# Optimization experiments

Measured on AMD Instinct MI355X. Metric: run time of the kernel, lower is better.

The kernel has to match this reference:

```python
import jax, jax.numpy as jnp
import numpy as np

IN_C, OUT_C, K, UP, C_DIM = 128, 64, 3, 2, 512
CLAMP = 256.0
ACT_GAIN = np.sqrt(2.0)  # lrelu def_gain


def _upfirdn_up2(x, f2):
    """upfirdn2d with up=2, padding=(3,2,3,2), gain=up^2 for a 4-tap filter.

    Padding values come from conv2d_resample: p = k//2 = 1, fw = 4, up = 2 =>
    px0 = p + (fw+up-1)//2 = 3, px1 = p + (fw-up)//2 = 2.
    """
    N, C, H, W = x.shape
    px0, px1 = 3, 2
    # zero-insert upsample (interior padding) fused with edge padding;
    # trailing zero of the up-sampled signal folded into the high pad.
    x = jax.lax.pad(x, jnp.asarray(0, x.dtype),
                    ((0, 0, 0), (0, 0, 0),
                     (px0, px1 + (UP - 1), UP - 1),
                     (px0, px1 + (UP - 1), UP - 1)))
    k = (f2 * (UP * UP)).astype(x.dtype)[None, None]   # [1,1,4,4], symmetric -> flip is a no-op
    k = jnp.tile(k, (C, 1, 1, 1))                       # depthwise FIR
    return jax.lax.conv_general_dilated(
        x, k, window_strides=(1, 1), padding='VALID',
        feature_group_count=C, dimension_numbers=('NCHW', 'OIHW', 'NCHW'))


def setup_inputs() -> dict:
    key = jax.random.key(0)
    ks = jax.random.split(key, 4)
    return {
        "x": jax.random.normal(ks[0], (8, IN_C, 128, 128), jnp.float32),
        "c": jax.random.normal(ks[1], (8, C_DIM), jnp.float32),
        "weight": jax.random.normal(ks[2], (OUT_C, IN_C, K, K), jnp.float32),
        "bias": jnp.zeros((OUT_C,), jnp.float32),
        "w_affine": jax.random.normal(ks[3], (IN_C, C_DIM), jnp.float32),
        "b_affine": jnp.zeros((IN_C,), jnp.float32),
    }


def reference(x, c, weight, bias, w_affine, b_affine):
    # setup_filter: normalize separable FIR taps
    f1 = jnp.array([1.0, 3.0, 3.0, 1.0], jnp.float32)
    f1 = f1 / jnp.sum(f1)
    f2 = jnp.outer(f1, f1)

    # hyper modulation: x *= 1 + tanh(affine(c))
    y = c @ (w_affine * (1.0 / np.sqrt(C_DIM))).T + b_affine   # FullyConnectedLayer, linear
    x = x * (1.0 + jnp.tanh(y))[:, :, None, None]

    # conv2d_resample(up=2, padding=k//2, flip_weight=False)
    w = weight * (1.0 / np.sqrt(IN_C * K * K))                  # weight_gain
    x = _upfirdn_up2(x, f2)                                      # [N,C,2H+2,2W+2]
    w = w[:, :, ::-1, ::-1]                                      # flip_weight=False => true convolution
    x = jax.lax.conv_general_dilated(
        x, w.astype(x.dtype), window_strides=(1, 1), padding='VALID',
        dimension_numbers=('NCHW', 'OIHW', 'NCHW'))              # [N,OUT_C,2H,2W]

    # bias_act: lrelu(x+b)*sqrt(2), clamp at +-256 (gain=1)
    x = jax.nn.leaky_relu(x + bias[None, :, None, None], 0.2) * ACT_GAIN
    return jnp.clip(x, -CLAMP, CLAMP)
```

## Files before the change

### kernel.cpp

```cpp
#include <hip/hip_runtime.h>
#include <math.h>

#define IN_C   128
#define OUT_C  64
#define CDIM   512
#define HW     128
#define PHW    130
#define OHW    256
#define NB     8

typedef __attribute__((ext_vector_type(8))) short short8;
typedef __attribute__((ext_vector_type(4))) float f32x4;

__device__ inline unsigned short f2bf(float f) {
    unsigned int u = __float_as_uint(f);
    unsigned int r = (u + 0x7fffu + ((u >> 16) & 1u)) >> 16;
    return (unsigned short)r;
}

__device__ inline float postact(float v) {
    v = v > 0.f ? v : 0.2f * v;
    v *= 1.4142135623730951f;
    return fminf(fmaxf(v, -256.f), 256.f);
}

__device__ __forceinline__ void gload16(const void* g, void* l) {
    __builtin_amdgcn_global_load_lds(
        (const __attribute__((address_space(1))) unsigned int*)g,
        (__attribute__((address_space(3))) unsigned int*)l, 16, 0, 0);
}

__global__ void gain_kernel(const float* __restrict__ c,
                            const float* __restrict__ w_affine,
                            const float* __restrict__ b_affine,
                            float* __restrict__ gain) {
    int wave = (blockIdx.x * blockDim.x + threadIdx.x) >> 6;
    int lane = threadIdx.x & 63;
    if (wave >= NB * IN_C) return;
    int n  = wave >> 7;
    int ic = wave & 127;
    const float* cp = c + n * CDIM;
    const float* wp = w_affine + ic * CDIM;
    float s = 0.f;
    #pragma unroll
    for (int k = 0; k < CDIM / 64; ++k) s += cp[lane + 64 * k] * wp[lane + 64 * k];
    #pragma unroll
    for (int off = 32; off > 0; off >>= 1) s += __shfl_down(s, off);
    if (lane == 0) {
        float y = s * 0.04419417382415922f + b_affine[ic];
        gain[n * IN_C + ic] = 1.0f + tanhf(y);
    }
}

__global__ void wbprep2_kernel(const float* __restrict__ w, unsigned short* __restrict__ wb2) {
    int idx = blockIdx.x * blockDim.x + threadIdx.x;
    if (idx >= 18 * 16384) return;
    int e    = idx & 7;
    int lane = (idx >> 3) & 63;
    int m16  = (idx >> 9) & 15;
    int kc   = (idx >> 13) & 1;
    int kt   = idx >> 14;
    int tap = kt >> 1, h = kt & 1;
    int m  = m16 * 16 + (lane & 15);
    int ic = h * 64 + kc * 32 + (lane >> 4) * 8 + e;
    int ky = tap / 3, kx = tap % 3;
    int oc = m >> 2, ph = m & 3;
    int py = ph >> 1, px = ph & 1;
    int sy = 2 * ky + (py == 0 ? 1 : 0);
    int sx = 2 * kx + (px == 0 ? 1 : 0);
    const float k1[4] = {0.25f, 0.75f, 0.75f, 0.25f};
    float sum = 0.f;
    #pragma unroll
    for (int by = 0; by < 3; ++by) {
        int ay = sy - by;
        if (ay < 0 || ay > 3) continue;
        #pragma unroll
        for (int bx = 0; bx < 3; ++bx) {
            int ax = sx - bx;
            if (ax < 0 || ax > 3) continue;
            sum += w[((oc * IN_C + ic) * 3 + (2 - by)) * 3 + (2 - bx)] * k1[ay] * k1[ax];
        }
    }
    wb2[idx] = f2bf(sum * 0.029462782549439483f);
}

__global__ __launch_bounds__(256) void xprep_kernel(const float* __restrict__ x,
                                                    const float* __restrict__ gain,
                                                    unsigned short* __restrict__ xg) {
    int n = blockIdx.x >> 7;
    int y = blockIdx.x & 127;
    __shared__ unsigned short lds[128][130];
    int tid = threadIdx.x;
    for (int i = tid; i < 128 * 128; i += 256) {
        int ic = i >> 7, pix = i & 127;
        float v = x[(((n * IN_C + ic) * HW) + y) * HW + pix] * gain[n * IN_C + ic];
        lds[pix][ic] = f2bf(v);
    }
    __syncthreads();
    unsigned int* dst = (unsigned int*)(xg + (((size_t)(n * PHW) + y + 1) * PHW + 1) * 128);
    for (int i = tid; i < 8192; i += 256) {
        int pix = i >> 6, d = i & 63;
        dst[pix * 64 + d] = *reinterpret_cast<const unsigned int*>(&lds[pix][d * 2]);
    }
}

__global__ void border_kernel(unsigned short* __restrict__ xg) {
    int id = blockIdx.x * blockDim.x + threadIdx.x;
    int c = id & 15;
    int t = id >> 4;
    int p = t % 516;
    int n = t / 516;
    if (n >= NB) return;
    int Y, X;
    if (p < 130)      { Y = 0;   X = p; }
    else if (p < 260) { Y = 129; X = p - 130; }
    else              { int q = p - 260; Y = 1 + (q >> 1); X = (q & 1) * 129; }
    uint4 z = make_uint4(0, 0, 0, 0);
    *reinterpret_cast<uint4*>(xg + (((size_t)(n * PHW) + Y) * PHW + X) * 128 + c * 8) = z;
}

#define BARRIER() do { __builtin_amdgcn_sched_barrier(0); __builtin_amdgcn_s_barrier(); __builtin_amdgcn_sched_barrier(0); } while (0)
#define MM(ACC, AF, BF) ACC = __builtin_amdgcn_mfma_f32_16x16x32_bf16(AF, BF, ACC, 0, 0, 0)

__global__ __launch_bounds__(512) void conv_mfma2(
    const unsigned short* __restrict__ xg,
    const unsigned short* __restrict__ wb2,
    const float* __restrict__ bias,
    float* __restrict__ out) {
    __shared__ __align__(16) char smem[131072];

    const int bid = blockIdx.x;
    const int n     = bid >> 6;
    const int patch = bid & 63;
    const int y0 = (patch >> 3) * 16;
    const int x0 = (patch & 7) * 16;
    const int tid  = threadIdx.x;
    const int lane = tid & 63;
    const int wid  = tid >> 6;
    const int wM = wid >> 2;
    const int wN = wid & 3;
    const int l16 = lane & 15;
    const int lhi = lane >> 4;
    const int mbase = wM * 8;
    const int pbase = wN * 4;

    int ldsoff[4]; int aoff[4]; size_t boff[4];
    #pragma unroll
    for (int r = 0; r < 4; ++r) {
        int slot = r * 512 + tid;
        ldsoff[r] = (r * 512 + wid * 64) * 16;
        aoff[r] = slot * 8;
        int px = slot >> 3, j = slot & 7, s = j ^ (px & 7);
        boff[r] = (((size_t)(n * PHW) + y0 + (px >> 4)) * PHW + (x0 + (px & 15))) * 128 + s * 8;
    }

    auto stage = [&](int k, int p) {
        int tap = k >> 1, h = k & 1;
        int ky = tap / 3, kx = tap - ky * 3;
        int toff = (ky * PHW + kx) * 128 + h * 64;
        const unsigned short* aS = wb2 + k * 16384;
        char* bufA = smem + (p << 16);
        #pragma unroll
        for (int r = 0; r < 4; ++r) gload16(aS + aoff[r], bufA + ldsoff[r]);
        #pragma unroll
        for (int r = 0; r < 4; ++r) gload16(xg + boff[r] + toff, bufA + 32768 + ldsoff[r]);
    };

    f32x4 acc[8][4];
    #pragma unroll
    for (int f = 0; f < 8; ++f)
        #pragma unroll
        for (int b = 0; b < 4; ++b) acc[f][b] = (f32x4)0.f;

    stage(0, 0);
    stage(1, 1);

    #pragma unroll 1
    for (int t = 0; t < 18; ++t) {
        const int p = t & 1;
        const char* bA = smem + (p << 16);
        const char* bB = bA + 32768;

        if (t >= 1 && t < 17) stage(t + 1, (t + 1) & 1);
        if (t < 17) { asm volatile("s_waitcnt vmcnt(8)" ::: "memory"); }
        else        { asm volatile("s_waitcnt vmcnt(0)" ::: "memory"); }
        BARRIER();

        auto ldA = [&](int f, int kc) -> short8 {
            return *reinterpret_cast<const short8*>(bA + (((kc << 4) + mbase + f) << 10) + (lane << 4));
        };
        auto ldB = [&](int b, int kc) -> short8 {
            int px = ((pbase + b) << 4) + l16;
            int off = (((kc << 6) + (lhi << 4)) ^ ((px & 7) << 4));
            return *reinterpret_cast<const short8*>(bB + (px << 7) + off);
        };

        short8 A0[4][2], A1[4][2], B0[2][2], B1[2][2];

        #pragma unroll
        for (int f = 0; f < 4; ++f) { A0[f][0] = ldA(f, 0); A0[f][1] = ldA(f, 1); }
        #pragma unroll
        for (int b = 0; b < 2; ++b) { B0[b][0] = ldB(b, 0); B0[b][1] = ldB(b, 1); }
        BARRIER();
        __builtin_amdgcn_s_setprio(1);
        #pragma unroll
        for (int f = 0; f < 4; ++f)
            #pragma unroll
            for (int b = 0; b < 2; ++b) { MM(acc[f][b], A0[f][0], B0[b][0]); MM(acc[f][b], A0[f][1], B0[b][1]); }
        __builtin_amdgcn_s_setprio(0);
        BARRIER();

        #pragma unroll
        for (int b = 0; b < 2; ++b) { B1[b][0] = ldB(b + 2, 0); B1[b][1] = ldB(b + 2, 1); }
        BARRIER();
        __builtin_amdgcn_s_setprio(1);
        #pragma unroll
        for (int f = 0; f < 4; ++f)
            #pragma unroll
            for (int b = 0; b < 2; ++b) { MM(acc[f][b + 2], A0[f][0], B1[b][0]); MM(acc[f][b + 2], A0[f][1], B1[b][1]); }
        __builtin_amdgcn_s_setprio(0);
        BARRIER();

        #pragma unroll
        for (int f = 0; f < 4; ++f) { A1[f][0] = ldA(4 + f, 0); A1[f][1] = ldA(4 + f, 1); }
        BARRIER();
        __builtin_amdgcn_s_setprio(1);
        #pragma unroll
        for (int f = 0; f < 4; ++f)
            #pragma unroll
            for (int b = 0; b < 2; ++b) { MM(acc[4 + f][b], A1[f][0], B0[b][0]); MM(acc[4 + f][b], A1[f][1], B0[b][1]); }
        __builtin_amdgcn_s_setprio(0);
        BARRIER();

        __builtin_amdgcn_s_setprio(1);
        #pragma unroll
        for (int f = 0; f < 4; ++f)
            #pragma unroll
            for (int b = 0; b < 2; ++b) { MM(acc[4 + f][b + 2], A1[f][0], B1[b][0]); MM(acc[4 + f][b + 2], A1[f][1], B1[b][1]); }
        __builtin_amdgcn_s_setprio(0);
        BARRIER();
    }

    #pragma unroll
    for (int f = 0; f < 8; ++f) {
        const int oc = wM * 32 + f * 4 + lhi;
        const float bi = bias[oc];
        #pragma unroll
        for (int b = 0; b < 4; ++b) {
            const int ypix = y0 + pbase + b;
            const int xpix = x0 + l16;
            float* o0 = out + (((size_t)(n * OUT_C + oc) * OHW) + 2 * ypix) * OHW + 2 * xpix;
            float2 v0 = make_float2(postact(acc[f][b][0] + bi), postact(acc[f][b][1] + bi));
            float2 v1 = make_float2(postact(acc[f][b][2] + bi), postact(acc[f][b][3] + bi));
            *reinterpret_cast<float2*>(o0) = v0;
            *reinterpret_cast<float2*>(o0 + OHW) = v1;
        }
    }
}

__global__ void wprep_kernel(const float* __restrict__ w, float* __restrict__ wp) {
    int idx = blockIdx.x * blockDim.x + threadIdx.x;
    if (idx >= IN_C * 9 * 4 * OUT_C) return;
    int oc = idx & 63;
    int t  = idx >> 6;
    int ph = t & 3;  t >>= 2;
    int kx = t % 3;  t /= 3;
    int ky = t % 3;  t /= 3;
    int ic = t;
    int py = ph >> 1, px = ph & 1;
    int sy = 2 * ky + (py == 0 ? 1 : 0);
    int sx = 2 * kx + (px == 0 ? 1 : 0);
    const float k1[4] = {0.25f, 0.75f, 0.75f, 0.25f};
    float sum = 0.f;
    #pragma unroll
    for (int by = 0; by < 3; ++by) {
        int ay = sy - by;
        if (ay < 0 || ay > 3) continue;
        #pragma unroll
        for (int bx = 0; bx < 3; ++bx) {
            int ax = sx - bx;
            if (ax < 0 || ax > 3) continue;
            sum += w[((oc * IN_C + ic) * 3 + (2 - by)) * 3 + (2 - bx)] * k1[ay] * k1[ax];
        }
    }
    wp[idx] = sum * 0.029462782549439483f;
}

__global__ __launch_bounds__(256) void conv_main(
    const float* __restrict__ x, const float* __restrict__ gain,
    const float* __restrict__ wp, const float* __restrict__ bias,
    float* __restrict__ out) {
    const int n    = blockIdx.z >> 3;
    const int occ  = (blockIdx.z & 7) * 8;
    const int tx0  = blockIdx.x * 16;
    const int ty0  = blockIdx.y * 16;
    const int tid  = threadIdx.x;
    const int lx   = tid & 15;
    const int ly   = tid >> 4;
    __shared__ float xsf[8][18][18];
    float acc[4][8];
    #pragma unroll
    for (int p = 0; p < 4; ++p)
        #pragma unroll
        for (int o = 0; o < 8; ++o) acc[p][o] = 0.f;
    for (int ic0 = 0; ic0 < IN_C; ic0 += 8) {
        __syncthreads();
        for (int i = tid; i < 8 * 324; i += 256) {
            int icb = i / 324;
            int rem = i - icb * 324;
            int yy  = rem / 18;
            int xx  = rem - yy * 18;
            int gy  = ty0 + yy - 1;
            int gx  = tx0 + xx - 1;
            int ic  = ic0 + icb;
            float v = 0.f;
            if (gy >= 0 && gy < HW && gx >= 0 && gx < HW)
                v = x[((n * IN_C + ic) * HW + gy) * HW + gx] * gain[n * IN_C + ic];
            xsf[icb][yy][xx] = v;
        }
        __syncthreads();
        for (int icb = 0; icb < 8; ++icb) {
            const int ic = ic0 + icb;
            const float* wpp = wp + ic * (9 * 4 * OUT_C) + occ;
            #pragma unroll
            for (int ky = 0; ky < 3; ++ky)
                #pragma unroll
                for (int kx = 0; kx < 3; ++kx) {
                    float tv = xsf[icb][ly + ky][lx + kx];
                    const float* w9 = wpp + (ky * 3 + kx) * (4 * OUT_C);
                    #pragma unroll
                    for (int p = 0; p < 4; ++p)
                        #pragma unroll
                        for (int o = 0; o < 8; ++o)
                            acc[p][o] = fmaf(tv, w9[p * OUT_C + o], acc[p][o]);
                }
        }
    }
    const int ybase = 2 * (ty0 + ly);
    const int xbase = 2 * (tx0 + lx);
    #pragma unroll
    for (int o = 0; o < 8; ++o) {
        float b = bias[occ + o];
        #pragma unroll
        for (int py = 0; py < 2; ++py) {
            float2 v;
            v.x = postact(acc[py * 2 + 0][o] + b);
            v.y = postact(acc[py * 2 + 1][o] + b);
            *reinterpret_cast<float2*>(
                &out[((size_t)(n * OUT_C + occ + o) * OHW + (ybase + py)) * OHW + xbase]) = v;
        }
    }
}

extern "C" void kernel_launch(void* const* d_in, const int* in_sizes, int n_in,
                              void* d_out, int out_size, void* d_ws, size_t ws_size,
                              hipStream_t stream) {
    const float* x        = (const float*)d_in[0];
    const float* c        = (const float*)d_in[1];
    const float* weight   = (const float*)d_in[2];
    const float* bias     = (const float*)d_in[3];
    const float* w_affine = (const float*)d_in[4];
    const float* b_affine = (const float*)d_in[5];
    float* out = (float*)d_out;

    float* gain = (float*)d_ws;

    const size_t NEED = 1048576 + (size_t)NB * PHW * PHW * IN_C * 2;
    if (ws_size >= NEED) {
        unsigned short* wb2 = (unsigned short*)((char*)d_ws + 8192);
        unsigned short* xg  = (unsigned short*)((char*)d_ws + 1048576);
        gain_kernel<<<dim3((NB * IN_C * 64) / 256), dim3(256), 0, stream>>>(c, w_affine, b_affine, gain);
        wbprep2_kernel<<<dim3((18 * 16384) / 256), dim3(256), 0, stream>>>(weight, wb2);
        xprep_kernel<<<dim3(NB * HW), dim3(256), 0, stream>>>(x, gain, xg);
        border_kernel<<<dim3((NB * 516 * 16) / 256), dim3(256), 0, stream>>>(xg);
        conv_mfma2<<<dim3(512), dim3(512), 0, stream>>>(xg, wb2, bias, out);
    } else {
        float* wp = (float*)((char*)d_ws + 8192);
        gain_kernel<<<dim3((NB * IN_C * 64) / 256), dim3(256), 0, stream>>>(c, w_affine, b_affine, gain);
        wprep_kernel<<<dim3((IN_C * 9 * 4 * OUT_C + 255) / 256), dim3(256), 0, stream>>>(weight, wp);
        conv_main<<<dim3(HW / 16, HW / 16, NB * 8), dim3(256), 0, stream>>>(x, gain, wp, bias, out);
    }
}
```

Measured before the change: 116.9 us.

## Load whole input halo tile into LDS once and stream only weights per tap

The conv kernel now copies the full 18x18 pixel by 128-channel input halo tile into LDS once at the start, instead of re-fetching a shifted activation tile from global memory for each of the 18 tap/half steps. Only the weight slabs stay double-buffered per step. xprep now writes the activation layout pre-swizzled so the LDS reads avoid bank conflicts. The inner loop is simplified to two k-chunks per step with fewer barriers. This cuts repeated global and L2 traffic for activations, but raises LDS use to about 145 KB and adds a large serial prologue before any MFMA work starts.

```diff
diff --git a/kernel.cpp b/kernel.cpp
--- a/kernel.cpp
+++ b/kernel.cpp
@@ -100,7 +100,9 @@
     unsigned int* dst = (unsigned int*)(xg + (((size_t)(n * PHW) + y + 1) * PHW + 1) * 128);
     for (int i = tid; i < 8192; i += 256) {
         int pix = i >> 6, d = i & 63;
-        dst[pix * 64 + d] = *reinterpret_cast<const unsigned int*>(&lds[pix][d * 2]);
+        int j = d >> 2, w = d & 3;
+        int js = j ^ ((pix + 1) & 7);
+        dst[pix * 64 + js * 4 + w] = *reinterpret_cast<const unsigned int*>(&lds[pix][d * 2]);
     }
 }
 
@@ -122,18 +124,18 @@
 #define BARRIER() do { __builtin_amdgcn_sched_barrier(0); __builtin_amdgcn_s_barrier(); __builtin_amdgcn_sched_barrier(0); } while (0)
 #define MM(ACC, AF, BF) ACC = __builtin_amdgcn_mfma_f32_16x16x32_bf16(AF, BF, ACC, 0, 0, 0)
 
-__global__ __launch_bounds__(512) void conv_mfma2(
+__global__ __launch_bounds__(512) void conv_mfma3(
     const unsigned short* __restrict__ xg,
     const unsigned short* __restrict__ wb2,
     const float* __restrict__ bias,
     float* __restrict__ out) {
-    __shared__ __align__(16) char smem[131072];
-
-    const int bid = blockIdx.x;
+    __shared__ __align__(16) char smem[148480];
+
+    const int bid   = blockIdx.x;
     const int n     = bid >> 6;
     const int patch = bid & 63;
-    const int y0 = (patch >> 3) * 16;
-    const int x0 = (patch & 7) * 16;
+    const int Y0 = (patch >> 3) * 16;
+    const int X0 = (patch & 7) * 16;
     const int tid  = threadIdx.x;
     const int lane = tid & 63;
     const int wid  = tid >> 6;
@@ -144,26 +146,26 @@
     const int mbase = wM * 8;
     const int pbase = wN * 4;
 
-    int ldsoff[4]; int aoff[4]; size_t boff[4];
-    #pragma unroll
-    for (int r = 0; r < 4; ++r) {
-        int slot = r * 512 + tid;
-        ldsoff[r] = (r * 512 + wid * 64) * 16;
-        aoff[r] = slot * 8;
-        int px = slot >> 3, j = slot & 7, s = j ^ (px & 7);
-        boff[r] = (((size_t)(n * PHW) + y0 + (px >> 4)) * PHW + (x0 + (px & 15))) * 128 + s * 8;
-    }
-
-    auto stage = [&](int k, int p) {
-        int tap = k >> 1, h = k & 1;
-        int ky = tap / 3, kx = tap - ky * 3;
-        int toff = (ky * PHW + kx) * 128 + h * 64;
-        const unsigned short* aS = wb2 + k * 16384;
-        char* bufA = smem + (p << 16);
-        #pragma unroll
-        for (int r = 0; r < 4; ++r) gload16(aS + aoff[r], bufA + ldsoff[r]);
-        #pragma unroll
-        for (int r = 0; r < 4; ++r) gload16(xg + boff[r] + toff, bufA + 32768 + ldsoff[r]);
+    const char* xgb  = (const char*)xg + (size_t)n * PHW * PHW * 256;
+    const char* wb2b = (const char*)wb2;
+
+    #pragma unroll 1
+    for (int i = 0; i < 11; ++i) {
+        int c = i * 512 + tid;
+        if (c < 5184) {
+            int r = c / 288;
+            int t = c - r * 288;
+            gload16(xgb + ((size_t)(Y0 + r) * PHW + X0) * 256 + t * 16,
+                    smem + 65536 + (i * 512 + wid * 64) * 16);
+        }
+    }
+
+    auto stageA = [&](int k, int p) {
+        const char* aS = wb2b + k * 32768;
+        char* buf = smem + (p << 15);
+        #pragma unroll
+        for (int r = 0; r < 4; ++r)
+            gload16(aS + (r * 512 + tid) * 16, buf + (r * 512 + wid * 64) * 16);
     };
 
     f32x4 acc[8][4];
@@ -172,17 +174,19 @@
         #pragma unroll
         for (int b = 0; b < 4; ++b) acc[f][b] = (f32x4)0.f;
 
-    stage(0, 0);
-    stage(1, 1);
+    stageA(0, 0);
+    stageA(1, 1);
 
     #pragma unroll 1
     for (int t = 0; t < 18; ++t) {
-        const int p = t & 1;
-        const char* bA = smem + (p << 16);
-        const char* bB = bA + 32768;
-
-        if (t >= 1 && t < 17) stage(t + 1, (t + 1) & 1);
-        if (t < 17) { asm volatile("s_waitcnt vmcnt(8)" ::: "memory"); }
+        const int p   = t & 1;
+        const int tap = t >> 1;
+        const int h   = t & 1;
+        const int ky  = tap / 3;
+        const int kx  = tap - ky * 3;
+        const char* bA = smem + (p << 15);
+
+        if (t < 17) { asm volatile("s_waitcnt vmcnt(4)" ::: "memory"); }
         else        { asm volatile("s_waitcnt vmcnt(0)" ::: "memory"); }
         BARRIER();
 
@@ -190,55 +194,30 @@
             return *reinterpret_cast<const short8*>(bA + (((kc << 4) + mbase + f) << 10) + (lane << 4));
         };
         auto ldB = [&](int b, int kc) -> short8 {
-            int px = ((pbase + b) << 4) + l16;
-            int off = (((kc << 6) + (lhi << 4)) ^ ((px & 7) << 4));
-            return *reinterpret_cast<const short8*>(bB + (px << 7) + off);
+            int R = pbase + b + ky;
+            int C = l16 + kx;
+            int icoff = (h << 7) + (kc << 6) + (lhi << 4);
+            return *reinterpret_cast<const short8*>(
+                smem + 65536 + (R * 18 + C) * 256 + (icoff ^ ((C & 7) << 4)));
         };
 
-        short8 A0[4][2], A1[4][2], B0[2][2], B1[2][2];
-
-        #pragma unroll
-        for (int f = 0; f < 4; ++f) { A0[f][0] = ldA(f, 0); A0[f][1] = ldA(f, 1); }
-        #pragma unroll
-        for (int b = 0; b < 2; ++b) { B0[b][0] = ldB(b, 0); B0[b][1] = ldB(b, 1); }
+        #pragma unroll
+        for (int kc = 0; kc < 2; ++kc) {
+            short8 Af[8], Bf[4];
+            #pragma unroll
+            for (int f = 0; f < 8; ++f) Af[f] = ldA(f, kc);
+            #pragma unroll
+            for (int b = 0; b < 4; ++b) Bf[b] = ldB(b, kc);
+            __builtin_amdgcn_s_setprio(1);
+            #pragma unroll
+            for (int f = 0; f < 8; ++f)
+                #pragma unroll
+                for (int b = 0; b < 4; ++b) MM(acc[f][b], Af[f], Bf[b]);
+            __builtin_amdgcn_s_setprio(0);
+        }
+
         BARRIER();
-        __builtin_amdgcn_s_setprio(1);
-        #pragma unroll
-        for (int f = 0; f < 4; ++f)
-            #pragma unroll
-            for (int b = 0; b < 2; ++b) { MM(acc[f][b], A0[f][0], B0[b][0]); MM(acc[f][b], A0[f][1], B0[b][1]); }
-        __builtin_amdgcn_s_setprio(0);
-        BARRIER();
-
-        #pragma unroll
-        for (int b = 0; b < 2; ++b) { B1[b][0] = ldB(b + 2, 0); B1[b][1] = ldB(b + 2, 1); }
-        BARRIER();
-        __builtin_amdgcn_s_setprio(1);
-        #pragma unroll
-        for (int f = 0; f < 4; ++f)
-            #pragma unroll
-            for (int b = 0; b < 2; ++b) { MM(acc[f][b + 2], A0[f][0], B1[b][0]); MM(acc[f][b + 2], A0[f][1], B1[b][1]); }
-        __builtin_amdgcn_s_setprio(0);
-        BARRIER();
-
-        #pragma unroll
-        for (int f = 0; f < 4; ++f) { A1[f][0] = ldA(4 + f, 0); A1[f][1] = ldA(4 + f, 1); }
-        BARRIER();
-        __builtin_amdgcn_s_setprio(1);
-        #pragma unroll
-        for (int f = 0; f < 4; ++f)
-            #pragma unroll
-            for (int b = 0; b < 2; ++b) { MM(acc[4 + f][b], A1[f][0], B0[b][0]); MM(acc[4 + f][b], A1[f][1], B0[b][1]); }
-        __builtin_amdgcn_s_setprio(0);
-        BARRIER();
-
-        __builtin_amdgcn_s_setprio(1);
-        #pragma unroll
-        for (int f = 0; f < 4; ++f)
-            #pragma unroll
-            for (int b = 0; b < 2; ++b) { MM(acc[4 + f][b + 2], A1[f][0], B1[b][0]); MM(acc[4 + f][b + 2], A1[f][1], B1[b][1]); }
-        __builtin_amdgcn_s_setprio(0);
-        BARRIER();
+        if (t + 2 < 18) stageA(t + 2, p);
     }
 
     #pragma unroll
@@ -247,8 +226,8 @@
         const float bi = bias[oc];
         #pragma unroll
         for (int b = 0; b < 4; ++b) {
-            const int ypix = y0 + pbase + b;
-            const int xpix = x0 + l16;
+            const int ypix = Y0 + pbase + b;
+            const int xpix = X0 + l16;
             float* o0 = out + (((size_t)(n * OUT_C + oc) * OHW) + 2 * ypix) * OHW + 2 * xpix;
             float2 v0 = make_float2(postact(acc[f][b][0] + bi), postact(acc[f][b][1] + bi));
             float2 v1 = make_float2(postact(acc[f][b][2] + bi), postact(acc[f][b][3] + bi));
@@ -373,7 +352,7 @@
         wbprep2_kernel<<<dim3((18 * 16384) / 256), dim3(256), 0, stream>>>(weight, wb2);
         xprep_kernel<<<dim3(NB * HW), dim3(256), 0, stream>>>(x, gain, xg);
         border_kernel<<<dim3((NB * 516 * 16) / 256), dim3(256), 0, stream>>>(xg);
-        conv_mfma2<<<dim3(512), dim3(512), 0, stream>>>(xg, wb2, bias, out);
+        conv_mfma3<<<dim3(512), dim3(512), 0, stream>>>(xg, wb2, bias, out);
     } else {
         float* wp = (float*)((char*)d_ws + 8192);
         gain_kernel<<<dim3((NB * IN_C * 64) / 256), dim3(256), 0, stream>>>(c, w_affine, b_affine, gain);
```

New measurement: 111.6 us. 1.05x faster.
